# Kernel optimization log

Hardware: AMD Instinct MI355X
Metric: run time of the kernel (lower is better)

Reference implementation:

```python
import jax, jax.numpy as jnp
import numpy as np

N, E, C, NEL, NB, G = 8192, 131072, 64, 10, 8, 32
RMAX, P, AVG, CORR, H = 5.0, 5, 16.0, 3, 16
L_OF = np.array([0, 1, 1, 1, 2, 2, 2, 2, 2, 3, 3, 3, 3, 3, 3, 3])  # l of each lm slot


def _sph(u):
    # real spherical harmonics l=0..3, e3nn 'component' normalization (|Y_l|^2 = 2l+1)
    x, y, z = u[:, 0], u[:, 1], u[:, 2]
    s3, s15 = jnp.sqrt(3.0), jnp.sqrt(15.0)
    Y = [jnp.ones_like(x),
         s3 * x, s3 * y, s3 * z,
         s15 * x * y, s15 * y * z, jnp.sqrt(1.25) * (3 * z * z - 1.0), s15 * x * z,
         jnp.sqrt(3.75) * (x * x - y * y),
         jnp.sqrt(35.0 / 8) * y * (3 * x * x - y * y), jnp.sqrt(105.0) * x * y * z,
         jnp.sqrt(21.0 / 8) * y * (5 * z * z - 1.0), jnp.sqrt(1.75) * z * (5 * z * z - 3.0),
         jnp.sqrt(21.0 / 8) * x * (5 * z * z - 1.0), jnp.sqrt(105.0 / 4) * z * (x * x - y * y),
         jnp.sqrt(35.0 / 8) * x * (x * x - 3 * y * y)]
    return jnp.stack(Y, axis=-1)  # [E,16]


def _radial(r):
    # Bessel basis * polynomial cutoff envelope (MACE RadialEmbeddingBlock)
    n = jnp.arange(1, NB + 1, dtype=r.dtype)
    rb = jnp.sqrt(2.0 / RMAX) * jnp.sin(n * jnp.pi * r[:, None] / RMAX) / r[:, None]
    x = r / RMAX
    env = 1.0 - 0.5 * (P + 1) * (P + 2) * x ** P + P * (P + 2) * x ** (P + 1) - 0.5 * P * (P + 1) * x ** (P + 2)
    env = jnp.where(x < 1.0, env, 0.0)
    return rb * env[:, None]  # [E,NB]


def setup_inputs():
    key = jax.random.key(0)
    ks = jax.random.split(key, 32)
    elems = jax.random.randint(ks[0], (N,), 0, NEL)
    node_attrs = jax.nn.one_hot(elems, NEL, dtype=jnp.float32)
    positions = jax.random.normal(ks[1], (N, 3), jnp.float32) * 2.0
    edge_index = jax.random.randint(ks[2], (2, E), 0, N)
    shifts = jnp.zeros((E, 3), jnp.float32)
    batch = jnp.sort(jax.random.randint(ks[3], (N,), 0, G))
    charges = jax.random.normal(ks[4], (N,), jnp.float32) * 0.1

    def nrm(k, shape, fan):
        return jax.random.normal(k, shape, jnp.float32) / np.sqrt(fan)

    params = dict(
        W_embed=nrm(ks[5], (NEL, C), NEL),
        Wr1a=nrm(ks[6], (NB, 64), NB), Wr1b=nrm(ks[7], (64, 4 * C), 64),
        Wmix1=nrm(ks[8], (4, C, C), C), Wsc1=nrm(ks[9], (NEL, C, C), C),
        Wprod1s=nrm(ks[10], (CORR, NEL, C), 1.0), Wprod1v=nrm(ks[11], (CORR, NEL, C), 1.0),
        Wp1_0=nrm(ks[12], (C, C), C), Wp1_1=nrm(ks[13], (C, C), C),
        w_read1=nrm(ks[14], (C,), C),
        Wr2a=nrm(ks[15], (NB, 64), NB), Wr2b=nrm(ks[16], (64, 4 * C), 64),
        Wmix2=nrm(ks[17], (4, C, C), C), Wsc2=nrm(ks[18], (NEL, C, C), C),
        Wprod2=nrm(ks[19], (CORR, NEL, C), 1.0), Wp2=nrm(ks[20], (C, C), C),
        Wv=nrm(ks[21], (C, H), C),
        Wg1=nrm(ks[22], (H, H), H), bg1=jnp.zeros((H,), jnp.float32),
        Wg2=nrm(ks[23], (H, H), H), bg2=jnp.zeros((H,), jnp.float32),
        w_read2=nrm(ks[24], (H,), H),
    )
    inp = dict(node_attrs=node_attrs, positions=positions, shifts=shifts, charges=charges,
               edge_index=edge_index, batch=batch, num_graphs=G)
    inp.update(params)
    return inp


def _forward(node_attrs, positions, shifts, charges, W_embed, Wr1a, Wr1b, Wmix1, Wsc1,
             Wprod1s, Wprod1v, Wp1_0, Wp1_1, w_read1, Wr2a, Wr2b, Wmix2, Wsc2, Wprod2,
             Wp2, Wv, Wg1, bg1, Wg2, bg2, w_read2, edge_index, batch, num_graphs):
    snd, rcv = edge_index[0], edge_index[1]
    vec = positions[rcv] - positions[snd] + shifts          # [E,3]
    r = jnp.sqrt(jnp.sum(vec * vec, -1) + 1e-12)
    u = vec / r[:, None]
    Y = _sph(u)                                              # [E,16]
    rb = _radial(r)                                          # [E,NB]

    h0 = node_attrs @ W_embed                                # node embedding [N,C]

    # ---- interaction 1: scalar node feats x SH, radial-weighted, scatter to receivers ----
    wr = (jax.nn.silu(rb @ Wr1a) @ Wr1b).reshape(E, 4, C)[:, L_OF, :]   # [E,16,C]
    M = h0[snd][:, None, :] * Y[:, :, None] * wr             # [E,16,C] edge messages
    A = jax.ops.segment_sum(M, rcv, num_segments=N) / AVG    # [N,16,C]
    h1 = jnp.einsum('nkc,kcd->nkd', A, Wmix1[L_OF])          # per-l linear mix
    sc1 = jnp.einsum('nk,nc,kcd->nd', node_attrs, h0, Wsc1)  # element-dep skip (scalar)

    # ---- product basis 1 (correlation-3, element-dependent polynomial contraction) ----
    ws = jnp.einsum('nk,pkc->pnc', node_attrs, Wprod1s)
    wv = jnp.einsum('nk,pkc->pnc', node_attrs, Wprod1v)
    s = h1[:, 0, :]
    m0 = sum(ws[p] * s ** (p + 1) for p in range(CORR))
    gv = sum(wv[p] * s ** p for p in range(CORR))
    out0 = m0 @ Wp1_0 + sc1                                  # [N,C] scalars
    out1 = jnp.einsum('nmc,cd->nmd', h1[:, 1:4, :] * gv[:, None, :], Wp1_1)  # [N,3,C]
    d1 = jnp.einsum('nmc,c->nm', out1, w_read1)              # linear dipole readout

    # ---- interaction 2 ----
    wr2 = (jax.nn.silu(rb @ Wr2a) @ Wr2b).reshape(E, 4, C)[:, L_OF, :]
    M2 = out0[snd][:, None, :] * Y[:, :, None] * wr2
    A2 = jax.ops.segment_sum(M2, rcv, num_segments=N) / AVG
    h2 = jnp.einsum('nkc,kcd->nkd', A2, Wmix2[L_OF])
    sc2 = jnp.einsum('nk,nmc,kcd->nmd', node_attrs, out1, Wsc2)
    wv2 = jnp.einsum('nk,pkc->pnc', node_attrs, Wprod2)
    s2 = h2[:, 0, :]
    gv2 = sum(wv2[p] * s2 ** p for p in range(CORR))
    out2 = jnp.einsum('nmc,cd->nmd', h2[:, 1:4, :] * gv2[:, None, :], Wp2) + sc2  # [N,3,C]

    # ---- nonlinear dipole readout (gated, invariant gates) ----
    vh = jnp.einsum('nmc,ch->nmh', out2, Wv)                 # [N,3,H]
    inv = jnp.sqrt(jnp.sum(vh * vh, axis=1) + 1e-12)         # invariant norms [N,H]
    a = jax.nn.silu(inv @ Wg1 + bg1) @ Wg2 + bg2
    d2 = jnp.einsum('nmh,nh,h->nm', vh, a, w_read2)

    atomic_dipoles = d1 + d2                                 # [N,3]
    total = jax.ops.segment_sum(atomic_dipoles, batch, num_segments=num_graphs)
    total = total + jax.ops.segment_sum(charges[:, None] * positions, batch, num_segments=num_graphs)
    return total, atomic_dipoles


def reference(node_attrs, positions, shifts, charges, W_embed, Wr1a, Wr1b, Wmix1, Wsc1,
              Wprod1s, Wprod1v, Wp1_0, Wp1_1, w_read1, Wr2a, Wr2b, Wmix2, Wsc2, Wprod2,
              Wp2, Wv, Wg1, bg1, Wg2, bg2, w_read2, edge_index, batch, num_graphs):
    return _forward(node_attrs, positions, shifts, charges, W_embed, Wr1a, Wr1b, Wmix1,
                    Wsc1, Wprod1s, Wprod1v, Wp1_0, Wp1_1, w_read1, Wr2a, Wr2b, Wmix2,
                    Wsc2, Wprod2, Wp2, Wv, Wg1, bg1, Wg2, bg2, w_read2, edge_index,
                    batch, num_graphs)
```

## Files before the change

### kernel.cpp

```cpp
#include <hip/hip_runtime.h>
#include <hip/hip_fp16.h>
#include <math.h>

#define NN 8192
#define EE 131072
#define CC 64
#define GG 32
#define NEL 10
#define NBLK2 522
#define NHB 32

__device__ __forceinline__ float silu_f(float x) { return x / (1.0f + __expf(-x)); }

typedef _Float16 h2v __attribute__((ext_vector_type(2)));
__device__ __forceinline__ float fdot2_u(unsigned int a, unsigned int b, float c) {
    return __builtin_amdgcn_fdot2(__builtin_bit_cast(h2v, a),
                                  __builtin_bit_cast(h2v, b), c, false);
}
__device__ __forceinline__ unsigned int pack_h2(float a, float b) {
    __half2 h = __floats2half2_rn(a, b);
    return *(unsigned int*)&h;
}

__device__ __forceinline__ void stage_wT(const float* __restrict__ W, float* sWT,
                                         int tid, int nt) {
    for (int idx = tid; idx < 4096; idx += nt) {
        int d = idx & 63, c = idx >> 6;
        sWT[(d << 6) + ((((c >> 2) ^ (d & 15)) << 2) | (c & 3))] = W[idx];
    }
}
#define WREAD(sWT, d, c4) (((const float4*)(sWT))[((d) << 4) + ((c4) ^ ((d) & 15))])
#define DOT4(a, b) ((a).x * (b).x + (a).y * (b).y + (a).z * (b).z + (a).w * (b).w)

__global__ __launch_bounds__(256) void k_h0(const float* __restrict__ na,
                                            const float* __restrict__ Wemb,
                                            float* __restrict__ h0,
                                            int* __restrict__ elem) {
    int n = blockIdx.x * 4 + (threadIdx.x >> 6);
    int d = threadIdx.x & 63;
    float acc = 0.0f;
    float best = -1.0f; int bi = 0;
    #pragma unroll
    for (int k = 0; k < NEL; k++) {
        float a = na[n * NEL + k];
        acc += a * Wemb[k * 64 + d];
        if (a > best) { best = a; bi = k; }
    }
    h0[n * 64 + d] = acc;
    if (d == 0) elem[n] = bi;
}

__global__ __launch_bounds__(256) void k_hist(const int* __restrict__ elem,
                                              int* __restrict__ bhist) {
    __shared__ int h[NEL];
    int t = threadIdx.x;
    if (t < NEL) h[t] = 0;
    __syncthreads();
    atomicAdd(&h[elem[blockIdx.x * 256 + t]], 1);
    __syncthreads();
    if (t < NEL) bhist[blockIdx.x * NEL + t] = h[t];
}

__global__ __launch_bounds__(256) void k_fill(const int* __restrict__ elem,
                                              const int* __restrict__ bbase2,
                                              int* __restrict__ order) {
    __shared__ int cur[NEL];
    int t = threadIdx.x;
    if (t < NEL) cur[t] = bbase2[blockIdx.x * NEL + t];
    __syncthreads();
    int n = blockIdx.x * 256 + t;
    int p = atomicAdd(&cur[elem[n]], 1);
    order[p] = n;
}

__global__ __launch_bounds__(64) void k_sc1tab(const float* __restrict__ Wemb,
                                               const float* __restrict__ Wsc1,
                                               float* __restrict__ tab) {
    int e = blockIdx.x, d = threadIdx.x;
    float acc = 0.0f;
    for (int c = 0; c < 64; c++)
        acc += Wemb[e * 64 + c] * Wsc1[e * 4096 + c * 64 + d];
    tab[e * 64 + d] = acc;
}

__device__ __forceinline__ int edge_live(const float* pos, const float* shifts,
                                         const int* eidx, int e, int* rcv_out) {
    int snd = eidx[e];
    int rcv = eidx[EE + e];
    float vx = pos[rcv * 3 + 0] - pos[snd * 3 + 0] + shifts[e * 3 + 0];
    float vy = pos[rcv * 3 + 1] - pos[snd * 3 + 1] + shifts[e * 3 + 1];
    float vz = pos[rcv * 3 + 2] - pos[snd * 3 + 2] + shifts[e * 3 + 2];
    float r = sqrtf(vx * vx + vy * vy + vz * vz + 1e-12f);
    *rcv_out = rcv;
    return (r * 0.2f) < 1.0f;
}
__global__ __launch_bounds__(256) void k_csr_count(const float* __restrict__ pos,
                                                   const float* __restrict__ shifts,
                                                   const int* __restrict__ eidx,
                                                   int* __restrict__ rowcnt) {
    int e = blockIdx.x * 256 + threadIdx.x;
    int rcv;
    if (edge_live(pos, shifts, eidx, e, &rcv)) atomicAdd(&rowcnt[rcv], 1);
}
__global__ __launch_bounds__(1024) void k_scan(const int* __restrict__ rowcnt,
                                               int* __restrict__ rowoff,
                                               int* __restrict__ rowcur,
                                               const int* __restrict__ bhist,
                                               int* __restrict__ bbase2,
                                               int* __restrict__ belem,
                                               int* __restrict__ bbase,
                                               int* __restrict__ blim) {
    __shared__ int part[1024];
    int t = threadIdx.x;
    if (t < NBLK2) belem[t] = -1;
    int loc[8]; int s = 0;
    #pragma unroll
    for (int k = 0; k < 8; k++) { loc[k] = rowcnt[t * 8 + k]; s += loc[k]; }
    part[t] = s;
    __syncthreads();
    for (int d = 1; d < 1024; d <<= 1) {
        int v = (t >= d) ? part[t - d] : 0;
        __syncthreads();
        part[t] += v;
        __syncthreads();
    }
    int run = (t > 0) ? part[t - 1] : 0;
    #pragma unroll
    for (int k = 0; k < 8; k++) {
        rowoff[t * 8 + k] = run; rowcur[t * 8 + k] = run; run += loc[k];
    }
    if (t == 1023) rowoff[8192] = run;
    __syncthreads();
    if (t == 0) {
        int s2 = 0, b = 0;
        for (int e = 0; e < NEL; e++) {
            int c = 0;
            int run2 = s2;
            for (int b2 = 0; b2 < NHB; b2++) {
                bbase2[b2 * NEL + e] = run2;
                int v = bhist[b2 * NEL + e];
                run2 += v; c += v;
            }
            for (int q = 0; q < c; q += 16) {
                belem[b] = e;
                bbase[b] = s2 + q;
                blim[b] = s2 + ((q + 16 < c) ? (q + 16) : c);
                b++;
            }
            s2 += c;
        }
    }
}
__global__ __launch_bounds__(256) void k_csr_fill(const float* __restrict__ pos,
                                                  const float* __restrict__ shifts,
                                                  const int* __restrict__ eidx,
                                                  int* __restrict__ rowcur,
                                                  int* __restrict__ elist) {
    int e = blockIdx.x * 256 + threadIdx.x;
    int rcv;
    if (edge_live(pos, shifts, eidx, e, &rcv)) {
        int p = atomicAdd(&rowcur[rcv], 1);
        elist[p] = e;
    }
}

__global__ __launch_bounds__(256) void edge_mlp(
    const float* __restrict__ feats, const float* __restrict__ pos,
    const float* __restrict__ shifts, const int* __restrict__ eidx,
    const int* __restrict__ elist, const int* __restrict__ rowoff,
    const float* __restrict__ Wra, const float* __restrict__ Wrb,
    unsigned int* __restrict__ msg, float4* __restrict__ ue4)
{
    int nlive = rowoff[NN];
    int e_base = blockIdx.x * 64;
    if (e_base >= nlive) return;

    __shared__ float smem[7424];
    __shared__ int   sSnd[64];
    float* sWaT = smem;
    unsigned int* sWbT = (unsigned int*)(smem + 512);
    __half* sMsgH = (__half*)smem;
    float* sRb = smem + 4608;
    unsigned int* sHidT = (unsigned int*)(smem + 5120);

    int tid = threadIdx.x;

    if (tid < 64) {
        int idx = e_base + tid;
        int ok = idx < nlive;
        int e = ok ? elist[idx] : elist[nlive - 1];
        int snd = eidx[e];
        int rcv = eidx[EE + e];
        float vx = pos[rcv * 3 + 0] - pos[snd * 3 + 0] + shifts[e * 3 + 0];
        float vy = pos[rcv * 3 + 1] - pos[snd * 3 + 1] + shifts[e * 3 + 1];
        float vz = pos[rcv * 3 + 2] - pos[snd * 3 + 2] + shifts[e * 3 + 2];
        float r = sqrtf(vx * vx + vy * vy + vz * vz + 1e-12f);
        float rinv = 1.0f / r;
        float x = r * 0.2f;
        float x2 = x * x, x4 = x2 * x2, x5 = x4 * x;
        float env = 1.0f - 21.0f * x5 + 35.0f * x5 * x - 15.0f * x5 * x2;
        float pref = ok ? 0.632455532033676f * rinv * env : 0.0f;
        float s1, c1;
        __sincosf(0.62831853071795865f * r, &s1, &c1);
        float k2c = 2.0f * c1;
        float sp = 0.0f, sn = s1;
        #pragma unroll
        for (int b = 0; b < 8; b++) {
            sRb[b * 64 + tid] = pref * sn;
            float t = k2c * sn - sp; sp = sn; sn = t;
        }
        if (ok) ue4[idx] = make_float4(vx * rinv, vy * rinv, vz * rinv, 0.0f);
        sSnd[tid] = snd;
    }
    for (int idx = tid; idx < 512; idx += 256) {
        int b = idx >> 6, j = idx & 63;
        sWaT[j * 8 + b] = Wra[idx];
    }
    for (int idx = tid; idx < 4096; idx += 256) {
        int c = idx & 127, j2 = idx >> 7;
        float s = (c < 64) ? 0.0625f : 0.10825317547305482f;
        float v0 = Wrb[(2 * j2) * 256 + c] * s;
        float v1 = Wrb[(2 * j2 + 1) * 256 + c] * s;
        int sj2 = (((j2 >> 2) ^ ((c >> 3) & 7)) << 2) | (j2 & 3);
        sWbT[c * 32 + sj2] = pack_h2(v0, v1);
    }
    __syncthreads();

    {
        int e = tid & 63, jg = tid >> 6;
        float rbv[8];
        #pragma unroll
        for (int b = 0; b < 8; b++) rbv[b] = sRb[b * 64 + e];
        const float4* waT4 = (const float4*)sWaT;
        float hid[16];
        #pragma unroll
        for (int jj = 0; jj < 16; jj++) {
            int j = jg * 16 + jj;
            float4 wa0 = waT4[j * 2 + 0];
            float4 wa1 = waT4[j * 2 + 1];
            float acc = rbv[0] * wa0.x + rbv[1] * wa0.y + rbv[2] * wa0.z + rbv[3] * wa0.w
                      + rbv[4] * wa1.x + rbv[5] * wa1.y + rbv[6] * wa1.z + rbv[7] * wa1.w;
            hid[jj] = silu_f(acc);
        }
        uint4* hidT4 = (uint4*)sHidT;
        uint4 u0, u1;
        u0.x = pack_h2(hid[0], hid[1]);  u0.y = pack_h2(hid[2], hid[3]);
        u0.z = pack_h2(hid[4], hid[5]);  u0.w = pack_h2(hid[6], hid[7]);
        u1.x = pack_h2(hid[8], hid[9]);  u1.y = pack_h2(hid[10], hid[11]);
        u1.z = pack_h2(hid[12], hid[13]); u1.w = pack_h2(hid[14], hid[15]);
        hidT4[e * 9 + jg * 2 + 0] = u0;
        hidT4[e * 9 + jg * 2 + 1] = u1;
    }
    __syncthreads();

    int cg = tid & 15, eg = tid >> 4;
    int e0 = eg * 4, c0 = cg * 8, cgl = cg & 7;
    const uint4* hidT4c = (const uint4*)sHidT;
    const uint4* wbT4 = (const uint4*)sWbT;
    float acc[4][8];
    #pragma unroll
    for (int i = 0; i < 4; i++)
        #pragma unroll
        for (int cc = 0; cc < 8; cc++) acc[i][cc] = 0.0f;

    for (int jc = 0; jc < 8; ++jc) {
        uint4 h0_ = hidT4c[(e0 + 0) * 9 + jc];
        uint4 h1_ = hidT4c[(e0 + 1) * 9 + jc];
        uint4 h2_ = hidT4c[(e0 + 2) * 9 + jc];
        uint4 h3_ = hidT4c[(e0 + 3) * 9 + jc];
        int wj = jc ^ cgl;
        #pragma unroll
        for (int cc = 0; cc < 8; cc++) {
            uint4 b = wbT4[(c0 + cc) * 8 + wj];
            acc[0][cc] = fdot2_u(h0_.x, b.x, acc[0][cc]);
            acc[0][cc] = fdot2_u(h0_.y, b.y, acc[0][cc]);
            acc[0][cc] = fdot2_u(h0_.z, b.z, acc[0][cc]);
            acc[0][cc] = fdot2_u(h0_.w, b.w, acc[0][cc]);
            acc[1][cc] = fdot2_u(h1_.x, b.x, acc[1][cc]);
            acc[1][cc] = fdot2_u(h1_.y, b.y, acc[1][cc]);
            acc[1][cc] = fdot2_u(h1_.z, b.z, acc[1][cc]);
            acc[1][cc] = fdot2_u(h1_.w, b.w, acc[1][cc]);
            acc[2][cc] = fdot2_u(h2_.x, b.x, acc[2][cc]);
            acc[2][cc] = fdot2_u(h2_.y, b.y, acc[2][cc]);
            acc[2][cc] = fdot2_u(h2_.z, b.z, acc[2][cc]);
            acc[2][cc] = fdot2_u(h2_.w, b.w, acc[2][cc]);
            acc[3][cc] = fdot2_u(h3_.x, b.x, acc[3][cc]);
            acc[3][cc] = fdot2_u(h3_.y, b.y, acc[3][cc]);
            acc[3][cc] = fdot2_u(h3_.z, b.z, acc[3][cc]);
            acc[3][cc] = fdot2_u(h3_.w, b.w, acc[3][cc]);
        }
    }
    __syncthreads();

    {
        uint4* msgT4 = (uint4*)sMsgH;
        #pragma unroll
        for (int i = 0; i < 4; ++i) {
            int e = e0 + i;
            int chunk = cg ^ (e & 15);
            uint4 u;
            u.x = pack_h2(acc[i][0], acc[i][1]);
            u.y = pack_h2(acc[i][2], acc[i][3]);
            u.z = pack_h2(acc[i][4], acc[i][5]);
            u.w = pack_h2(acc[i][6], acc[i][7]);
            msgT4[e * 18 + chunk] = u;
        }
    }
    __syncthreads();

    {
        int q = tid >> 6, c = tid & 63;
        #pragma unroll 4
        for (int i = 0; i < 16; ++i) {
            int e = q * 16 + i;
            int idx = e_base + e;
            if (idx >= nlive) continue;
            int snd = sSnd[e];
            float f = feats[(size_t)snd * CC + c];
            int xk = e & 15;
            float w0 = __half2float(sMsgH[e * 144 + ((((c >> 3)) ^ xk) << 3) + (c & 7)]);
            float w1 = __half2float(sMsgH[e * 144 + (((8 + (c >> 3)) ^ xk) << 3) + (c & 7)]);
            __half2 h = __floats2half2_rn(w0 * f, w1 * f);
            msg[(size_t)idx * 64 + c] = *(unsigned int*)&h;
        }
    }
}

__global__ __launch_bounds__(256) void k_gather(
    const int* __restrict__ rowoff,
    const unsigned int* __restrict__ msg, const float4* __restrict__ ue4,
    float* __restrict__ A)
{
    int n = blockIdx.x * 4 + (threadIdx.x >> 6);
    int d = threadIdx.x & 63;
    int s0 = rowoff[n], s1 = rowoff[n + 1];
    float a0 = 0.f, ax = 0.f, ay = 0.f, az = 0.f;
    for (int s = s0; s < s1; ++s) {
        unsigned int mu = msg[(size_t)s * 64 + d];
        float4 u = ue4[s];
        float2 m = __half22float2(*(__half2*)&mu);
        a0 += m.x;
        ax = fmaf(m.y, u.x, ax);
        ay = fmaf(m.y, u.y, ay);
        az = fmaf(m.y, u.z, az);
    }
    float* Ar = A + (size_t)n * 256;
    Ar[d] = a0; Ar[64 + d] = ax; Ar[128 + d] = ay; Ar[192 + d] = az;
}

__global__ __launch_bounds__(256) void node1(
    const int* __restrict__ elem, const float* __restrict__ A,
    const float* __restrict__ Wmix1, const float* __restrict__ sc1tab,
    const float* __restrict__ Wp1s, const float* __restrict__ Wp1v,
    const float* __restrict__ Wp10, const float* __restrict__ Wp11,
    const float* __restrict__ wrd1,
    float* __restrict__ out0, float* __restrict__ out1, float* __restrict__ d1)
{
    __shared__ float smem[10240];
    float* sB0 = smem;
    float* sB1 = smem + 4096;
    float* sIn = smem + 8192;

    int tid = threadIdx.x, w = tid >> 6, d = tid & 63;
    stage_wT(Wmix1,        sB0, tid, 256);
    stage_wT(Wmix1 + 4096, sB1, tid, 256);
    int nbase = blockIdx.x * 8;
    for (int idx = tid; idx < 2048; idx += 256)
        sIn[idx] = A[(size_t)nbase * 256 + idx];
    __syncthreads();

    const float4* sIn4 = (const float4*)sIn;
    int rbase = w * 8;
    int nloc = nbase + w * 2;

    float accs[2] = {0.f, 0.f};
    float acch[2][3];
    #pragma unroll
    for (int i = 0; i < 2; i++) acch[i][0] = acch[i][1] = acch[i][2] = 0.f;

    #pragma unroll 4
    for (int c4 = 0; c4 < 16; ++c4) {
        float4 w0 = WREAD(sB0, d, c4);
        float4 w1 = WREAD(sB1, d, c4);
        #pragma unroll
        for (int i = 0; i < 2; ++i) {
            int rb = rbase + i * 4;
            float4 a0 = sIn4[(rb + 0) * 16 + c4];
            accs[i] += DOT4(a0, w0);
            float4 a1 = sIn4[(rb + 1) * 16 + c4]; acch[i][0] += DOT4(a1, w1);
            float4 a2 = sIn4[(rb + 2) * 16 + c4]; acch[i][1] += DOT4(a2, w1);
            float4 a3 = sIn4[(rb + 3) * 16 + c4]; acch[i][2] += DOT4(a3, w1);
        }
    }

    #pragma unroll
    for (int i = 0; i < 2; ++i) {
        int n = nloc + i, e = elem[n];
        float s = accs[i];
        float ws0 = Wp1s[e * 64 + d], ws1 = Wp1s[640 + e * 64 + d], ws2 = Wp1s[1280 + e * 64 + d];
        float wv0 = Wp1v[e * 64 + d], wv1 = Wp1v[640 + e * 64 + d], wv2 = Wp1v[1280 + e * 64 + d];
        float m0 = s * (ws0 + s * (ws1 + s * ws2));
        float gv = wv0 + s * (wv1 + s * wv2);
        int rb = rbase + i * 4;
        sIn[(rb + 0) * 64 + d] = m0;
        sIn[(rb + 1) * 64 + d] = acch[i][0] * gv;
        sIn[(rb + 2) * 64 + d] = acch[i][1] * gv;
        sIn[(rb + 3) * 64 + d] = acch[i][2] * gv;
    }
    __syncthreads();

    stage_wT(Wp10, sB0, tid, 256);
    stage_wT(Wp11, sB1, tid, 256);
    __syncthreads();

    float acc0[2] = {0.f, 0.f};
    float acc1[2][3];
    #pragma unroll
    for (int i = 0; i < 2; i++) acc1[i][0] = acc1[i][1] = acc1[i][2] = 0.f;

    #pragma unroll 4
    for (int c4 = 0; c4 < 16; ++c4) {
        float4 p0 = WREAD(sB0, d, c4);
        float4 p1 = WREAD(sB1, d, c4);
        #pragma unroll
        for (int i = 0; i < 2; ++i) {
            int rb = rbase + i * 4;
            float4 a0 = sIn4[(rb + 0) * 16 + c4];
            acc0[i] += DOT4(a0, p0);
            float4 a1 = sIn4[(rb + 1) * 16 + c4]; acc1[i][0] += DOT4(a1, p1);
            float4 a2 = sIn4[(rb + 2) * 16 + c4]; acc1[i][1] += DOT4(a2, p1);
            float4 a3 = sIn4[(rb + 3) * 16 + c4]; acc1[i][2] += DOT4(a3, p1);
        }
    }

    float wr = wrd1[d];
    #pragma unroll
    for (int i = 0; i < 2; ++i) {
        int n = nloc + i, e = elem[n];
        out0[(size_t)n * 64 + d] = acc0[i] + sc1tab[e * 64 + d];
        #pragma unroll
        for (int m = 0; m < 3; ++m) {
            float o = acc1[i][m];
            out1[((size_t)n * 3 + m) * 64 + d] = o;
            float v = o * wr;
            v += __shfl_xor(v, 32); v += __shfl_xor(v, 16); v += __shfl_xor(v, 8);
            v += __shfl_xor(v, 4);  v += __shfl_xor(v, 2);  v += __shfl_xor(v, 1);
            if (d == 0) d1[n * 3 + m] = v;
        }
    }
}

__global__ __launch_bounds__(512) void node2(
    const int* __restrict__ belem, const int* __restrict__ bbase,
    const int* __restrict__ blim, const int* __restrict__ order,
    const float* __restrict__ A, const float* __restrict__ out1,
    const float* __restrict__ d1,
    const float* __restrict__ Wmix2, const float* __restrict__ Wsc2,
    const float* __restrict__ Wpr2, const float* __restrict__ Wp2,
    const float* __restrict__ Wv, const float* __restrict__ Wg1,
    const float* __restrict__ bg1, const float* __restrict__ Wg2,
    const float* __restrict__ bg2, const float* __restrict__ wrd2,
    float* __restrict__ dip)
{
    int b = blockIdx.x;
    int e = belem[b];
    if (e < 0) return;
    int base = bbase[b];
    int nv = blim[b] - base;

    __shared__ float smem[13312];
    __shared__ int   sNid[16];
    __shared__ int   sVal[16];
    float* sB0 = smem;
    float* sB1 = smem + 4096;
    float* sWv = smem + 8192;
    float* sIn = smem + 9216;

    int tid = threadIdx.x, w = tid >> 6, d = tid & 63;
    if (tid < 16) {
        sVal[tid] = tid < nv;
        sNid[tid] = order[base + (tid < nv ? tid : nv - 1)];
    }
    stage_wT(Wmix2,        sB0, tid, 512);
    stage_wT(Wmix2 + 4096, sB1, tid, 512);
    for (int idx = tid; idx < 1024; idx += 512) {
        int h = idx & 15, c = idx >> 4;
        sWv[(h << 6) + ((((c >> 2) ^ h) << 2) | (c & 3))] = Wv[idx];
    }
    __syncthreads();
    for (int idx = tid; idx < 4096; idx += 512) {
        int row = idx >> 6, q = row >> 2, k = row & 3, dd = idx & 63;
        sIn[idx] = A[(size_t)sNid[q] * 256 + k * 64 + dd];
    }
    __syncthreads();

    const float4* sIn4 = (const float4*)sIn;
    int rbase = w * 8;

    float accs[2] = {0.f, 0.f};
    float acch[2][3];
    #pragma unroll
    for (int i = 0; i < 2; i++) acch[i][0] = acch[i][1] = acch[i][2] = 0.f;

    #pragma unroll 4
    for (int c4 = 0; c4 < 16; ++c4) {
        float4 w0 = WREAD(sB0, d, c4);
        float4 w1 = WREAD(sB1, d, c4);
        #pragma unroll
        for (int i = 0; i < 2; ++i) {
            int rb = rbase + i * 4;
            float4 a0 = sIn4[(rb + 0) * 16 + c4];
            accs[i] += DOT4(a0, w0);
            float4 a1 = sIn4[(rb + 1) * 16 + c4]; acch[i][0] += DOT4(a1, w1);
            float4 a2 = sIn4[(rb + 2) * 16 + c4]; acch[i][1] += DOT4(a2, w1);
            float4 a3 = sIn4[(rb + 3) * 16 + c4]; acch[i][2] += DOT4(a3, w1);
        }
    }

    float wp0 = Wpr2[e * 64 + d], wp1 = Wpr2[640 + e * 64 + d], wp2_ = Wpr2[1280 + e * 64 + d];
    #pragma unroll
    for (int i = 0; i < 2; ++i) {
        float s2 = accs[i];
        float gv2 = wp0 + s2 * (wp1 + s2 * wp2_);
        int rb = rbase + i * 4;
        sIn[(rb + 1) * 64 + d] = acch[i][0] * gv2;
        sIn[(rb + 2) * 64 + d] = acch[i][1] * gv2;
        sIn[(rb + 3) * 64 + d] = acch[i][2] * gv2;
    }
    __syncthreads();

    stage_wT(Wp2,             sB0, tid, 512);
    stage_wT(Wsc2 + e * 4096, sB1, tid, 512);
    __syncthreads();

    float acc2[2][3];
    #pragma unroll
    for (int i = 0; i < 2; i++) acc2[i][0] = acc2[i][1] = acc2[i][2] = 0.f;
    const float4* o14 = (const float4*)out1;

    #pragma unroll 4
    for (int c4 = 0; c4 < 16; ++c4) {
        float4 p = WREAD(sB0, d, c4);
        float4 s = WREAD(sB1, d, c4);
        #pragma unroll
        for (int i = 0; i < 2; ++i) {
            int rb = rbase + i * 4;
            size_t nq = (size_t)sNid[w * 2 + i];
            #pragma unroll
            for (int m = 0; m < 3; ++m) {
                float4 t  = sIn4[(rb + 1 + m) * 16 + c4];
                float4 o1 = o14[(nq * 3 + m) * 16 + c4];
                acc2[i][m] += DOT4(t, p) + DOT4(o1, s);
            }
        }
    }

    int m = d >> 4, h = d & 15;
    const float4* sWv4 = (const float4*)sWv;
    #pragma unroll
    for (int i = 0; i < 2; ++i) {
        int q = w * 2 + i, rb = rbase + i * 4;
        int n = sNid[q], valid = sVal[q];
        sIn[(rb + 1) * 64 + d] = acc2[i][0];
        sIn[(rb + 2) * 64 + d] = acc2[i][1];
        sIn[(rb + 3) * 64 + d] = acc2[i][2];

        float vh = 0.f;
        if (d < 48) {
            #pragma unroll 4
            for (int c4 = 0; c4 < 16; ++c4) {
                float4 o2 = sIn4[(rb + 1 + m) * 16 + c4];
                float4 wv = sWv4[(h << 4) + (c4 ^ h)];
                vh += DOT4(o2, wv);
            }
            sIn[rb * 64 + m * 16 + h] = vh;
        }
        float* g = sIn + rb * 64;
        if (d < 16) {
            float v0 = g[d], v1 = g[16 + d], v2 = g[32 + d];
            g[48 + d] = sqrtf(v0 * v0 + v1 * v1 + v2 * v2 + 1e-12f);
        }
        if (d < 16) {
            float acc = bg1[d];
            for (int k = 0; k < 16; ++k) acc += g[48 + k] * Wg1[k * 16 + d];
            g[48 + d] = silu_f(acc);
        }
        if (d < 16) {
            float acc = bg2[d];
            for (int k = 0; k < 16; ++k) acc += g[48 + k] * Wg2[k * 16 + d];
            g[48 + d] = acc * wrd2[d];
        }
        if (d < 48) {
            float v = vh * g[48 + h];
            v += __shfl_xor(v, 8, 16); v += __shfl_xor(v, 4, 16);
            v += __shfl_xor(v, 2, 16); v += __shfl_xor(v, 1, 16);
            if (h == 0 && valid)
                dip[n * 3 + m] = d1[n * 3 + m] + v;
        }
    }
}

__global__ __launch_bounds__(256) void k_total_part(
    const float* __restrict__ dip, const float* __restrict__ chg,
    const float* __restrict__ pos, const int* __restrict__ batch,
    float* __restrict__ wtotal)
{
    __shared__ float tot[GG * 3];
    int t = threadIdx.x;
    for (int i = t; i < GG * 3; i += 256) tot[i] = 0.f;
    __syncthreads();
    int n = blockIdx.x * 256 + t;
    int g = batch[n];
    float c = chg[n];
    atomicAdd(&tot[g * 3 + 0], dip[n * 3 + 0] + c * pos[n * 3 + 0]);
    atomicAdd(&tot[g * 3 + 1], dip[n * 3 + 1] + c * pos[n * 3 + 1]);
    atomicAdd(&tot[g * 3 + 2], dip[n * 3 + 2] + c * pos[n * 3 + 2]);
    __syncthreads();
    for (int i = t; i < GG * 3; i += 256) wtotal[blockIdx.x * (GG * 3) + i] = tot[i];
}
__global__ __launch_bounds__(96) void k_total_final(const float* __restrict__ wtotal,
                                                    float* __restrict__ total) {
    int i = threadIdx.x;
    float s = 0.f;
    for (int b = 0; b < NHB; b++) s += wtotal[b * (GG * 3) + i];
    total[i] = s;
}

extern "C" void kernel_launch(void* const* d_in, const int* in_sizes, int n_in,
                              void* d_out, int out_size, void* d_ws, size_t ws_size,
                              hipStream_t stream) {
    const float* na     = (const float*)d_in[0];
    const float* pos    = (const float*)d_in[1];
    const float* shifts = (const float*)d_in[2];
    const float* chg    = (const float*)d_in[3];
    const int*   eidx   = (const int*)d_in[4];
    const int*   batch  = (const int*)d_in[5];
    const float* Wemb   = (const float*)d_in[7];
    const float* Wr1a   = (const float*)d_in[8];
    const float* Wr1b   = (const float*)d_in[9];
    const float* Wmix1  = (const float*)d_in[10];
    const float* Wsc1   = (const float*)d_in[11];
    const float* Wp1s   = (const float*)d_in[12];
    const float* Wp1v   = (const float*)d_in[13];
    const float* Wp10   = (const float*)d_in[14];
    const float* Wp11   = (const float*)d_in[15];
    const float* wrd1   = (const float*)d_in[16];
    const float* Wr2a   = (const float*)d_in[17];
    const float* Wr2b   = (const float*)d_in[18];
    const float* Wmix2  = (const float*)d_in[19];
    const float* Wsc2   = (const float*)d_in[20];
    const float* Wpr2   = (const float*)d_in[21];
    const float* Wp2    = (const float*)d_in[22];
    const float* Wv     = (const float*)d_in[23];
    const float* Wg1    = (const float*)d_in[24];
    const float* bg1    = (const float*)d_in[25];
    const float* Wg2    = (const float*)d_in[26];
    const float* bg2    = (const float*)d_in[27];
    const float* wrd2   = (const float*)d_in[28];

    unsigned int* msg = (unsigned int*)d_ws;
    float4* ue4  = (float4*)(msg + (size_t)EE * 64);
    float* A     = (float*)(ue4 + EE);
    float* h0    = A + (size_t)NN * 4 * CC;
    float* out0  = h0 + (size_t)NN * CC;
    float* out1  = out0 + (size_t)NN * CC;
    float* d1    = out1 + (size_t)NN * 3 * CC;
    float* sc1t  = d1 + (size_t)NN * 3;
    float* wtotal= sc1t + NEL * 64;
    int* elem    = (int*)(wtotal + NHB * GG * 3);
    int* bhist   = elem + NN;
    int* bbase2  = bhist + NHB * NEL;
    int* rowcnt  = bbase2 + NHB * NEL;
    int* rowoff  = rowcnt + NN;
    int* rowcur  = rowoff + NN + 1;
    int* order   = rowcur + NN;
    int* elist   = order + NN;
    int* belem   = elist + EE;
    int* bbase   = belem + NBLK2;
    int* blim    = bbase + NBLK2;

    float* total = (float*)d_out;
    float* dip   = total + GG * 3;

    hipMemsetAsync(rowcnt, 0, (size_t)NN * sizeof(int), stream);

    k_h0<<<NN / 4, 256, 0, stream>>>(na, Wemb, h0, elem);
    k_csr_count<<<EE / 256, 256, 0, stream>>>(pos, shifts, eidx, rowcnt);
    k_hist<<<NHB, 256, 0, stream>>>(elem, bhist);
    k_scan<<<1, 1024, 0, stream>>>(rowcnt, rowoff, rowcur, bhist, bbase2,
                                   belem, bbase, blim);
    k_csr_fill<<<EE / 256, 256, 0, stream>>>(pos, shifts, eidx, rowcur, elist);
    k_fill<<<NHB, 256, 0, stream>>>(elem, bbase2, order);
    k_sc1tab<<<NEL, 64, 0, stream>>>(Wemb, Wsc1, sc1t);

    edge_mlp<<<EE / 64, 256, 0, stream>>>(h0, pos, shifts, eidx, elist, rowoff,
                                          Wr1a, Wr1b, msg, ue4);
    k_gather<<<NN / 4, 256, 0, stream>>>(rowoff, msg, ue4, A);
    node1<<<NN / 8, 256, 0, stream>>>(elem, A, Wmix1, sc1t, Wp1s, Wp1v, Wp10, Wp11,
                                      wrd1, out0, out1, d1);
    edge_mlp<<<EE / 64, 256, 0, stream>>>(out0, pos, shifts, eidx, elist, rowoff,
                                          Wr2a, Wr2b, msg, ue4);
    k_gather<<<NN / 4, 256, 0, stream>>>(rowoff, msg, ue4, A);
    node2<<<NBLK2, 512, 0, stream>>>(belem, bbase, blim, order, A, out1, d1,
                                     Wmix2, Wsc2, Wpr2, Wp2, Wv, Wg1, bg1,
                                     Wg2, bg2, wrd2, dip);
    k_total_part<<<NHB, 256, 0, stream>>>(dip, chg, pos, batch, wtotal);
    k_total_final<<<1, 96, 0, stream>>>(wtotal, total);
}
```

Measured before the change: 221.7 us.

## Store node features and weights in fp16 and use packed dot2 in node kernels

```diff
diff --git a/kernel.cpp b/kernel.cpp
--- a/kernel.cpp
+++ b/kernel.cpp
@@ -21,16 +21,22 @@
     __half2 h = __floats2half2_rn(a, b);
     return *(unsigned int*)&h;
 }
-
-__device__ __forceinline__ void stage_wT(const float* __restrict__ W, float* sWT,
-                                         int tid, int nt) {
-    for (int idx = tid; idx < 4096; idx += nt) {
-        int d = idx & 63, c = idx >> 6;
-        sWT[(d << 6) + ((((c >> 2) ^ (d & 15)) << 2) | (c & 3))] = W[idx];
-    }
-}
-#define WREAD(sWT, d, c4) (((const float4*)(sWT))[((d) << 4) + ((c4) ^ ((d) & 15))])
-#define DOT4(a, b) ((a).x * (b).x + (a).y * (b).y + (a).z * (b).z + (a).w * (b).w)
+__device__ __forceinline__ float dot8_u4(uint4 a, uint4 b, float c) {
+    c = fdot2_u(a.x, b.x, c); c = fdot2_u(a.y, b.y, c);
+    c = fdot2_u(a.z, b.z, c); c = fdot2_u(a.w, b.w, c);
+    return c;
+}
+
+__device__ __forceinline__ void stage_whT(const float* __restrict__ W,
+                                          unsigned int* sWh, int tid, int nt) {
+    for (int idx = tid; idx < 2048; idx += nt) {
+        int d = idx & 63, c2 = idx >> 6;
+        float v0 = W[(2 * c2) * 64 + d];
+        float v1 = W[(2 * c2 + 1) * 64 + d];
+        sWh[d * 36 + (((c2 >> 2) ^ (d & 7)) << 2) + (c2 & 3)] = pack_h2(v0, v1);
+    }
+}
+#define WH4(sWh, d, jc) (((const uint4*)(sWh))[(d) * 9 + ((jc) ^ ((d) & 7))])
 
 __global__ __launch_bounds__(256) void k_h0(const float* __restrict__ na,
                                             const float* __restrict__ Wemb,
@@ -272,22 +278,10 @@
         #pragma unroll
         for (int cc = 0; cc < 8; cc++) {
             uint4 b = wbT4[(c0 + cc) * 8 + wj];
-            acc[0][cc] = fdot2_u(h0_.x, b.x, acc[0][cc]);
-            acc[0][cc] = fdot2_u(h0_.y, b.y, acc[0][cc]);
-            acc[0][cc] = fdot2_u(h0_.z, b.z, acc[0][cc]);
-            acc[0][cc] = fdot2_u(h0_.w, b.w, acc[0][cc]);
-            acc[1][cc] = fdot2_u(h1_.x, b.x, acc[1][cc]);
-            acc[1][cc] = fdot2_u(h1_.y, b.y, acc[1][cc]);
-            acc[1][cc] = fdot2_u(h1_.z, b.z, acc[1][cc]);
-            acc[1][cc] = fdot2_u(h1_.w, b.w, acc[1][cc]);
-            acc[2][cc] = fdot2_u(h2_.x, b.x, acc[2][cc]);
-            acc[2][cc] = fdot2_u(h2_.y, b.y, acc[2][cc]);
-            acc[2][cc] = fdot2_u(h2_.z, b.z, acc[2][cc]);
-            acc[2][cc] = fdot2_u(h2_.w, b.w, acc[2][cc]);
-            acc[3][cc] = fdot2_u(h3_.x, b.x, acc[3][cc]);
-            acc[3][cc] = fdot2_u(h3_.y, b.y, acc[3][cc]);
-            acc[3][cc] = fdot2_u(h3_.z, b.z, acc[3][cc]);
-            acc[3][cc] = fdot2_u(h3_.w, b.w, acc[3][cc]);
+            acc[0][cc] = dot8_u4(h0_, b, acc[0][cc]);
+            acc[1][cc] = dot8_u4(h1_, b, acc[1][cc]);
+            acc[2][cc] = dot8_u4(h2_, b, acc[2][cc]);
+            acc[3][cc] = dot8_u4(h3_, b, acc[3][cc]);
         }
     }
     __syncthreads();
@@ -329,7 +323,7 @@
 __global__ __launch_bounds__(256) void k_gather(
     const int* __restrict__ rowoff,
     const unsigned int* __restrict__ msg, const float4* __restrict__ ue4,
-    float* __restrict__ A)
+    __half* __restrict__ Ah)
 {
     int n = blockIdx.x * 4 + (threadIdx.x >> 6);
     int d = threadIdx.x & 63;
@@ -344,32 +338,36 @@
         ay = fmaf(m.y, u.y, ay);
         az = fmaf(m.y, u.z, az);
     }
-    float* Ar = A + (size_t)n * 256;
-    Ar[d] = a0; Ar[64 + d] = ax; Ar[128 + d] = ay; Ar[192 + d] = az;
+    __half* Ar = Ah + (size_t)n * 256;
+    Ar[d] = __float2half(a0);
+    Ar[64 + d] = __float2half(ax);
+    Ar[128 + d] = __float2half(ay);
+    Ar[192 + d] = __float2half(az);
 }
 
 __global__ __launch_bounds__(256) void node1(
-    const int* __restrict__ elem, const float* __restrict__ A,
+    const int* __restrict__ elem, const unsigned int* __restrict__ AhU,
     const float* __restrict__ Wmix1, const float* __restrict__ sc1tab,
     const float* __restrict__ Wp1s, const float* __restrict__ Wp1v,
     const float* __restrict__ Wp10, const float* __restrict__ Wp11,
     const float* __restrict__ wrd1,
-    float* __restrict__ out0, float* __restrict__ out1, float* __restrict__ d1)
+    float* __restrict__ out0, __half* __restrict__ out1h, float* __restrict__ d1)
 {
-    __shared__ float smem[10240];
-    float* sB0 = smem;
-    float* sB1 = smem + 4096;
-    float* sIn = smem + 8192;
+    __shared__ unsigned int smem[5632];
+    unsigned int* sB0 = smem;
+    unsigned int* sB1 = smem + 2304;
+    unsigned int* sInH = smem + 4608;
 
     int tid = threadIdx.x, w = tid >> 6, d = tid & 63;
-    stage_wT(Wmix1,        sB0, tid, 256);
-    stage_wT(Wmix1 + 4096, sB1, tid, 256);
+    stage_whT(Wmix1,        sB0, tid, 256);
+    stage_whT(Wmix1 + 4096, sB1, tid, 256);
     int nbase = blockIdx.x * 8;
-    for (int idx = tid; idx < 2048; idx += 256)
-        sIn[idx] = A[(size_t)nbase * 256 + idx];
-    __syncthreads();
-
-    const float4* sIn4 = (const float4*)sIn;
+    for (int idx = tid; idx < 1024; idx += 256)
+        sInH[idx] = AhU[(size_t)nbase * 128 + idx];
+    __syncthreads();
+
+    const uint4* sInH4 = (const uint4*)sInH;
+    __half* sInHh = (__half*)sInH;
     int rbase = w * 8;
     int nloc = nbase + w * 2;
 
@@ -378,18 +376,16 @@
     #pragma unroll
     for (int i = 0; i < 2; i++) acch[i][0] = acch[i][1] = acch[i][2] = 0.f;
 
-    #pragma unroll 4
-    for (int c4 = 0; c4 < 16; ++c4) {
-        float4 w0 = WREAD(sB0, d, c4);
-        float4 w1 = WREAD(sB1, d, c4);
+    for (int jc = 0; jc < 8; ++jc) {
+        uint4 w0 = WH4(sB0, d, jc);
+        uint4 w1 = WH4(sB1, d, jc);
         #pragma unroll
         for (int i = 0; i < 2; ++i) {
             int rb = rbase + i * 4;
-            float4 a0 = sIn4[(rb + 0) * 16 + c4];
-            accs[i] += DOT4(a0, w0);
-            float4 a1 = sIn4[(rb + 1) * 16 + c4]; acch[i][0] += DOT4(a1, w1);
-            float4 a2 = sIn4[(rb + 2) * 16 + c4]; acch[i][1] += DOT4(a2, w1);
-            float4 a3 = sIn4[(rb + 3) * 16 + c4]; acch[i][2] += DOT4(a3, w1);
+            accs[i]    = dot8_u4(sInH4[(rb + 0) * 8 + jc], w0, accs[i]);
+            acch[i][0] = dot8_u4(sInH4[(rb + 1) * 8 + jc], w1, acch[i][0]);
+            acch[i][1] = dot8_u4(sInH4[(rb + 2) * 8 + jc], w1, acch[i][1]);
+            acch[i][2] = dot8_u4(sInH4[(rb + 3) * 8 + jc], w1, acch[i][2]);
         }
     }
 
@@ -402,15 +398,15 @@
         float m0 = s * (ws0 + s * (ws1 + s * ws2));
         float gv = wv0 + s * (wv1 + s * wv2);
         int rb = rbase + i * 4;
-        sIn[(rb + 0) * 64 + d] = m0;
-        sIn[(rb + 1) * 64 + d] = acch[i][0] * gv;
-        sIn[(rb + 2) * 64 + d] = acch[i][1] * gv;
-        sIn[(rb + 3) * 64 + d] = acch[i][2] * gv;
-    }
-    __syncthreads();
-
-    stage_wT(Wp10, sB0, tid, 256);
-    stage_wT(Wp11, sB1, tid, 256);
+        sInHh[(rb + 0) * 64 + d] = __float2half(m0);
+        sInHh[(rb + 1) * 64 + d] = __float2half(acch[i][0] * gv);
+        sInHh[(rb + 2) * 64 + d] = __float2half(acch[i][1] * gv);
+        sInHh[(rb + 3) * 64 + d] = __float2half(acch[i][2] * gv);
+    }
+    __syncthreads();
+
+    stage_whT(Wp10, sB0, tid, 256);
+    stage_whT(Wp11, sB1, tid, 256);
     __syncthreads();
 
     float acc0[2] = {0.f, 0.f};
@@ -418,18 +414,16 @@
     #pragma unroll
     for (int i = 0; i < 2; i++) acc1[i][0] = acc1[i][1] = acc1[i][2] = 0.f;
 
-    #pragma unroll 4
-    for (int c4 = 0; c4 < 16; ++c4) {
-        float4 p0 = WREAD(sB0, d, c4);
-        float4 p1 = WREAD(sB1, d, c4);
+    for (int jc = 0; jc < 8; ++jc) {
+        uint4 p0 = WH4(sB0, d, jc);
+        uint4 p1 = WH4(sB1, d, jc);
         #pragma unroll
         for (int i = 0; i < 2; ++i) {
             int rb = rbase + i * 4;
-            float4 a0 = sIn4[(rb + 0) * 16 + c4];
-            acc0[i] += DOT4(a0, p0);
-            float4 a1 = sIn4[(rb + 1) * 16 + c4]; acc1[i][0] += DOT4(a1, p1);
-            float4 a2 = sIn4[(rb + 2) * 16 + c4]; acc1[i][1] += DOT4(a2, p1);
-            float4 a3 = sIn4[(rb + 3) * 16 + c4]; acc1[i][2] += DOT4(a3, p1);
+            acc0[i]    = dot8_u4(sInH4[(rb + 0) * 8 + jc], p0, acc0[i]);
+            acc1[i][0] = dot8_u4(sInH4[(rb + 1) * 8 + jc], p1, acc1[i][0]);
+            acc1[i][1] = dot8_u4(sInH4[(rb + 2) * 8 + jc], p1, acc1[i][1]);
+            acc1[i][2] = dot8_u4(sInH4[(rb + 3) * 8 + jc], p1, acc1[i][2]);
         }
     }
 
@@ -441,7 +435,7 @@
         #pragma unroll
         for (int m = 0; m < 3; ++m) {
             float o = acc1[i][m];
-            out1[((size_t)n * 3 + m) * 64 + d] = o;
+            out1h[((size_t)n * 3 + m) * 64 + d] = __float2half(o);
             float v = o * wr;
             v += __shfl_xor(v, 32); v += __shfl_xor(v, 16); v += __shfl_xor(v, 8);
             v += __shfl_xor(v, 4);  v += __shfl_xor(v, 2);  v += __shfl_xor(v, 1);
@@ -453,7 +447,7 @@
 __global__ __launch_bounds__(512) void node2(
     const int* __restrict__ belem, const int* __restrict__ bbase,
     const int* __restrict__ blim, const int* __restrict__ order,
-    const float* __restrict__ A, const float* __restrict__ out1,
+    const unsigned int* __restrict__ AhU, const unsigned int* __restrict__ out1hU,
     const float* __restrict__ d1,
     const float* __restrict__ Wmix2, const float* __restrict__ Wsc2,
     const float* __restrict__ Wpr2, const float* __restrict__ Wp2,
@@ -468,33 +462,35 @@
     int base = bbase[b];
     int nv = blim[b] - base;
 
-    __shared__ float smem[13312];
-    __shared__ int   sNid[16];
-    __shared__ int   sVal[16];
-    float* sB0 = smem;
-    float* sB1 = smem + 4096;
-    float* sWv = smem + 8192;
-    float* sIn = smem + 9216;
+    __shared__ unsigned int smem[7232];
+    __shared__ int sNid[16];
+    __shared__ int sVal[16];
+    unsigned int* sB0 = smem;
+    unsigned int* sB1 = smem + 2304;
+    unsigned int* sWvH = smem + 4608;
+    unsigned int* sInH = smem + 5184;
 
     int tid = threadIdx.x, w = tid >> 6, d = tid & 63;
     if (tid < 16) {
         sVal[tid] = tid < nv;
         sNid[tid] = order[base + (tid < nv ? tid : nv - 1)];
     }
-    stage_wT(Wmix2,        sB0, tid, 512);
-    stage_wT(Wmix2 + 4096, sB1, tid, 512);
-    for (int idx = tid; idx < 1024; idx += 512) {
-        int h = idx & 15, c = idx >> 4;
-        sWv[(h << 6) + ((((c >> 2) ^ h) << 2) | (c & 3))] = Wv[idx];
-    }
-    __syncthreads();
-    for (int idx = tid; idx < 4096; idx += 512) {
-        int row = idx >> 6, q = row >> 2, k = row & 3, dd = idx & 63;
-        sIn[idx] = A[(size_t)sNid[q] * 256 + k * 64 + dd];
-    }
-    __syncthreads();
-
-    const float4* sIn4 = (const float4*)sIn;
+    stage_whT(Wmix2,        sB0, tid, 512);
+    stage_whT(Wmix2 + 4096, sB1, tid, 512);
+    for (int idx = tid; idx < 512; idx += 512) {
+        int h = idx & 15, c2 = idx >> 4;
+        sWvH[h * 36 + (((c2 >> 2) ^ (h & 7)) << 2) + (c2 & 3)] =
+            pack_h2(Wv[(2 * c2) * 16 + h], Wv[(2 * c2 + 1) * 16 + h]);
+    }
+    __syncthreads();
+    for (int idx = tid; idx < 2048; idx += 512) {
+        int q = idx >> 7, r = idx & 127;
+        sInH[idx] = AhU[(size_t)sNid[q] * 128 + r];
+    }
+    __syncthreads();
+
+    const uint4* sInH4 = (const uint4*)sInH;
+    __half* sInHh = (__half*)sInH;
     int rbase = w * 8;
 
     float accs[2] = {0.f, 0.f};
@@ -502,18 +498,16 @@
     #pragma unroll
     for (int i = 0; i < 2; i++) acch[i][0] = acch[i][1] = acch[i][2] = 0.f;
 
-    #pragma unroll 4
-    for (int c4 = 0; c4 < 16; ++c4) {
-        float4 w0 = WREAD(sB0, d, c4);
-        float4 w1 = WREAD(sB1, d, c4);
+    for (int jc = 0; jc < 8; ++jc) {
+        uint4 w0 = WH4(sB0, d, jc);
+        uint4 w1 = WH4(sB1, d, jc);
         #pragma unroll
         for (int i = 0; i < 2; ++i) {
             int rb = rbase + i * 4;
-            float4 a0 = sIn4[(rb + 0) * 16 + c4];
-            accs[i] += DOT4(a0, w0);
-            float4 a1 = sIn4[(rb + 1) * 16 + c4]; acch[i][0] += DOT4(a1, w1);
-            float4 a2 = sIn4[(rb + 2) * 16 + c4]; acch[i][1] += DOT4(a2, w1);
-            float4 a3 = sIn4[(rb + 3) * 16 + c4]; acch[i][2] += DOT4(a3, w1);
+            accs[i]    = dot8_u4(sInH4[(rb + 0) * 8 + jc], w0, accs[i]);
+            acch[i][0] = dot8_u4(sInH4[(rb + 1) * 8 + jc], w1, acch[i][0]);
+            acch[i][1] = dot8_u4(sInH4[(rb + 2) * 8 + jc], w1, acch[i][1]);
+            acch[i][2] = dot8_u4(sInH4[(rb + 3) * 8 + jc], w1, acch[i][2]);
         }
     }
 
@@ -523,80 +517,69 @@
         float s2 = accs[i];
         float gv2 = wp0 + s2 * (wp1 + s2 * wp2_);
         int rb = rbase + i * 4;
-        sIn[(rb + 1) * 64 + d] = acch[i][0] * gv2;
-        sIn[(rb + 2) * 64 + d] = acch[i][1] * gv2;
-        sIn[(rb + 3) * 64 + d] = acch[i][2] * gv2;
-    }
-    __syncthreads();
-
-    stage_wT(Wp2,             sB0, tid, 512);
-    stage_wT(Wsc2 + e * 4096, sB1, tid, 512);
+        sInHh[(rb + 1) * 64 + d] = __float2half(acch[i][0] * gv2);
+        sInHh[(rb + 2) * 64 + d] = __float2half(acch[i][1] * gv2);
+        sInHh[(rb + 3) * 64 + d] = __float2half(acch[i][2] * gv2);
+    }
+    __syncthreads();
+
+    stage_whT(Wp2,             sB0, tid, 512);
+    stage_whT(Wsc2 + e * 4096, sB1, tid, 512);
     __syncthreads();
 
     float acc2[2][3];
     #pragma unroll
     for (int i = 0; i < 2; i++) acc2[i][0] = acc2[i][1] = acc2[i][2] = 0.f;
-    const float4* o14 = (const float4*)out1;
-
-    #pragma unroll 4
-    for (int c4 = 0; c4 < 16; ++c4) {
-        float4 p = WREAD(sB0, d, c4);
-        float4 s = WREAD(sB1, d, c4);
+    const uint4* o1U4 = (const uint4*)out1hU;
+
+    for (int jc = 0; jc < 8; ++jc) {
+        uint4 p = WH4(sB0, d, jc);
+        uint4 s = WH4(sB1, d, jc);
         #pragma unroll
         for (int i = 0; i < 2; ++i) {
             int rb = rbase + i * 4;
             size_t nq = (size_t)sNid[w * 2 + i];
             #pragma unroll
             for (int m = 0; m < 3; ++m) {
-                float4 t  = sIn4[(rb + 1 + m) * 16 + c4];
-                float4 o1 = o14[(nq * 3 + m) * 16 + c4];
-                acc2[i][m] += DOT4(t, p) + DOT4(o1, s);
+                acc2[i][m] = dot8_u4(sInH4[(rb + 1 + m) * 8 + jc], p, acc2[i][m]);
+                acc2[i][m] = dot8_u4(o1U4[(nq * 3 + m) * 8 + jc], s, acc2[i][m]);
             }
         }
     }
 
     int m = d >> 4, h = d & 15;
-    const float4* sWv4 = (const float4*)sWv;
     #pragma unroll
     for (int i = 0; i < 2; ++i) {
         int q = w * 2 + i, rb = rbase + i * 4;
         int n = sNid[q], valid = sVal[q];
-        sIn[(rb + 1) * 64 + d] = acc2[i][0];
-        sIn[(rb + 2) * 64 + d] = acc2[i][1];
-        sIn[(rb + 3) * 64 + d] = acc2[i][2];
+        sInHh[(rb + 1) * 64 + d] = __float2half(acc2[i][0]);
+        sInHh[(rb + 2) * 64 + d] = __float2half(acc2[i][1]);
+        sInHh[(rb + 3) * 64 + d] = __float2half(acc2[i][2]);
 
         float vh = 0.f;
         if (d < 48) {
-            #pragma unroll 4
-            for (int c4 = 0; c4 < 16; ++c4) {
-                float4 o2 = sIn4[(rb + 1 + m) * 16 + c4];
-                float4 wv = sWv4[(h << 4) + (c4 ^ h)];
-                vh += DOT4(o2, wv);
+            for (int jc = 0; jc < 8; ++jc) {
+                uint4 o2 = sInH4[(rb + 1 + m) * 8 + jc];
+                uint4 wv = ((const uint4*)sWvH)[h * 9 + (jc ^ (h & 7))];
+                vh = dot8_u4(o2, wv, vh);
             }
-            sIn[rb * 64 + m * 16 + h] = vh;
-        }
-        float* g = sIn + rb * 64;
-        if (d < 16) {
-            float v0 = g[d], v1 = g[16 + d], v2 = g[32 + d];
-            g[48 + d] = sqrtf(v0 * v0 + v1 * v1 + v2 * v2 + 1e-12f);
-        }
-        if (d < 16) {
-            float acc = bg1[d];
-            for (int k = 0; k < 16; ++k) acc += g[48 + k] * Wg1[k * 16 + d];
-            g[48 + d] = silu_f(acc);
-        }
-        if (d < 16) {
-            float acc = bg2[d];
-            for (int k = 0; k < 16; ++k) acc += g[48 + k] * Wg2[k * 16 + d];
-            g[48 + d] = acc * wrd2[d];
-        }
-        if (d < 48) {
-            float v = vh * g[48 + h];
-            v += __shfl_xor(v, 8, 16); v += __shfl_xor(v, 4, 16);
-            v += __shfl_xor(v, 2, 16); v += __shfl_xor(v, 1, 16);
-            if (h == 0 && valid)
-                dip[n * 3 + m] = d1[n * 3 + m] + v;
-        }
+        }
+        float v1 = __shfl(vh, (d & 15) + 16);
+        float v2 = __shfl(vh, (d & 15) + 32);
+        float inv = sqrtf(vh * vh + v1 * v1 + v2 * v2 + 1e-12f);
+        float a1 = bg1[h];
+        #pragma unroll
+        for (int k = 0; k < 16; ++k) a1 += __shfl(inv, k) * Wg1[k * 16 + h];
+        float s1 = silu_f(a1);
+        float a2 = bg2[h];
+        #pragma unroll
+        for (int k = 0; k < 16; ++k) a2 += __shfl(s1, k) * Wg2[k * 16 + h];
+        float aw = a2 * wrd2[h];
+        float v = vh * aw;
+        v += __shfl_xor(v, 8, 16); v += __shfl_xor(v, 4, 16);
+        v += __shfl_xor(v, 2, 16); v += __shfl_xor(v, 1, 16);
+        if (d < 48 && h == 0 && valid)
+            dip[n * 3 + m] = d1[n * 3 + m] + v;
     }
 }
 
@@ -679,6 +662,11 @@
     int* bbase   = belem + NBLK2;
     int* blim    = bbase + NBLK2;
 
+    __half* Ah          = (__half*)A;
+    unsigned int* AhU   = (unsigned int*)A;
+    __half* out1h       = (__half*)out1;
+    unsigned int* out1hU= (unsigned int*)out1;
+
     float* total = (float*)d_out;
     float* dip   = total + GG * 3;
 
@@ -695,13 +683,13 @@
 
     edge_mlp<<<EE / 64, 256, 0, stream>>>(h0, pos, shifts, eidx, elist, rowoff,
                                           Wr1a, Wr1b, msg, ue4);
-    k_gather<<<NN / 4, 256, 0, stream>>>(rowoff, msg, ue4, A);
-    node1<<<NN / 8, 256, 0, stream>>>(elem, A, Wmix1, sc1t, Wp1s, Wp1v, Wp10, Wp11,
-                                      wrd1, out0, out1, d1);
+    k_gather<<<NN / 4, 256, 0, stream>>>(rowoff, msg, ue4, Ah);
+    node1<<<NN / 8, 256, 0, stream>>>(elem, AhU, Wmix1, sc1t, Wp1s, Wp1v, Wp10, Wp11,
+                                      wrd1, out0, out1h, d1);
     edge_mlp<<<EE / 64, 256, 0, stream>>>(out0, pos, shifts, eidx, elist, rowoff,
                                           Wr2a, Wr2b, msg, ue4);
-    k_gather<<<NN / 4, 256, 0, stream>>>(rowoff, msg, ue4, A);
-    node2<<<NBLK2, 512, 0, stream>>>(belem, bbase, blim, order, A, out1, d1,
+    k_gather<<<NN / 4, 256, 0, stream>>>(rowoff, msg, ue4, Ah);
+    node2<<<NBLK2, 512, 0, stream>>>(belem, bbase, blim, order, AhU, out1hU, d1,
                                      Wmix2, Wsc2, Wpr2, Wp2, Wv, Wg1, bg1,
                                      Wg2, bg2, wrd2, dip);
     k_total_part<<<NHB, 256, 0, stream>>>(dip, chg, pos, batch, wtotal);
```

Result: slower. 256.2 us (+15.6%).
